# Optimization experiments

Hardware: AMD Instinct MI355X
Metric: run time of the kernel (lower is better)

The kernel has to match this reference:

```python
import jax, jax.numpy as jnp
import numpy as np

B, S, D = 2, 2048, 2048
H, HD = 16, 128


def _rope_cos_sin(seq_len, head_dim, base=10000.0):
    inv_freq = 1.0 / (base ** (np.arange(0, head_dim, 2, dtype=np.float32) / head_dim))
    t = np.arange(seq_len, dtype=np.float32)
    freqs = np.outer(t, inv_freq)                      # [S, HD/2]
    emb = np.concatenate([freqs, freqs], axis=-1)      # [S, HD]
    return jnp.asarray(np.cos(emb)), jnp.asarray(np.sin(emb))


def setup_inputs() -> dict:
    key = jax.random.key(0)
    k1, k2, k3 = jax.random.split(key, 3)
    hidden_states = jax.random.normal(k1, (B, S, D), dtype=jnp.float32)
    cos, sin = _rope_cos_sin(S, HD)
    # qkv weight: [3, H*HD, D] as in CastedLinear(batch_output_dims=(3,))
    w_qkv = jax.random.normal(k2, (3, H * HD, D), dtype=jnp.float32) * (1.0 / D ** 0.5)
    w_o = jax.random.normal(k3, (D, H * HD), dtype=jnp.float32) * (1.0 / (H * HD) ** 0.5)
    return {"hidden_states": hidden_states, "cos": cos, "sin": sin, "w_qkv": w_qkv, "w_o": w_o}


def _rotate_half(x):
    x1, x2 = jnp.split(x, 2, axis=-1)
    return jnp.concatenate([-x2, x1], axis=-1)


def _apply_rope(x, cos, sin):
    # x: [B, S, H, HD]; cos/sin: [S, HD] -> broadcast over heads via [:, None, :]
    return x * cos[:, None, :] + _rotate_half(x) * sin[:, None, :]


def reference(hidden_states, cos, sin, w_qkv, w_o):
    # fused QKV projection: weight flattened to [3*H*HD, D]
    qkv = jnp.einsum('bsd,fd->bsf', hidden_states, w_qkv.reshape(-1, D))  # [B,S,3*H*HD]
    # rearrange '... (h hd) -> ... h hd' with h=H  ->  [B,S,H,3*HD], then chunk
    qkv = qkv.reshape(B, S, H, 3 * HD)
    q, k, v = jnp.split(qkv, 3, axis=-1)          # each [B,S,H,HD]
    q = _apply_rope(q, cos, sin)
    k = _apply_rope(k, cos, sin)
    # SDPA, causal
    scale = 1.0 / jnp.sqrt(jnp.asarray(HD, dtype=q.dtype))
    scores = jnp.einsum('bshd,bthd->bhst', q, k) * scale      # [B,H,S,S]
    causal = jnp.tril(jnp.ones((S, S), dtype=bool))
    scores = jnp.where(causal, scores, jnp.asarray(-jnp.inf, dtype=scores.dtype))
    probs = jax.nn.softmax(scores, axis=-1)
    attn = jnp.einsum('bhst,bthd->bshd', probs, v)            # [B,S,H,HD]
    attn = attn.reshape(B, S, H * HD)
    return jnp.einsum('bsf,df->bsd', attn, w_o)               # [B,S,D]
```

## Files before the change

### kernel.cpp

```cpp
#include <hip/hip_runtime.h>

typedef unsigned short u16;
typedef __bf16 bf16x8 __attribute__((ext_vector_type(8)));
typedef float f32x4 __attribute__((ext_vector_type(4)));


__device__ __forceinline__ u16 f2bf(float x) {
  __bf16 h = (__bf16)x;
  return __builtin_bit_cast(u16, h);
}

__device__ __forceinline__ void async_copy16(void* lds, const void* g) {
  __builtin_amdgcn_global_load_lds((const __attribute__((address_space(1))) void*)g,
                                   (__attribute__((address_space(3))) void*)lds, 16, 0, 0);
}

__global__ __launch_bounds__(256) void cast_all(const float* __restrict__ hidden,
                                                const float* __restrict__ wqkv,
                                                const float* __restrict__ wo,
                                                u16* __restrict__ xb,
                                                u16* __restrict__ wqb,
                                                u16* __restrict__ wob) {
  int i = blockIdx.x * 256 + threadIdx.x;
  const float* s;
  u16* d;
  int off;
  if (i < 2097152) { s = hidden; d = xb; off = i; }
  else if (i < 2097152 + 3145728) { s = wqkv; d = wqb; off = i - 2097152; }
  else { s = wo; d = wob; off = i - (2097152 + 3145728); }
  float4 v = ((const float4*)s)[off];
  ushort4 o;
  o.x = f2bf(v.x); o.y = f2bf(v.y); o.z = f2bf(v.z); o.w = f2bf(v.w);
  ((ushort4*)d)[off] = o;
}

__global__ __launch_bounds__(256) void gemm_qkv(const u16* __restrict__ A,
                                                const u16* __restrict__ W,
                                                const float* __restrict__ cosb,
                                                const float* __restrict__ sinb,
                                                u16* __restrict__ Qb,
                                                u16* __restrict__ Kb,
                                                u16* __restrict__ Vt) {
  __shared__ __align__(16) u16 As[128 * 64];
  __shared__ __align__(16) u16 Bs[128 * 64];
  const int tid = threadIdx.x;
  const int lane = tid & 63;
  const int wave = tid >> 6;
  const int wm = (wave >> 1) * 64;
  const int r16 = lane & 15;
  const int g4 = lane >> 4;
  const int rsw = r16 & 7;
  const int bm = blockIdx.x * 128;
  const int bn = blockIdx.y * 128;

  size_t aoff[4], boff[4];
  u16* ldsA[4];
  u16* ldsB[4];
#pragma unroll
  for (int i = 0; i < 4; i++) {
    int row = wave * 32 + i * 8 + (lane >> 3);
    int c = (lane & 7) ^ (row & 7);
    aoff[i] = (size_t)(bm + row) * 2048 + c * 8;
    boff[i] = (size_t)(bn + row) * 2048 + c * 8;
    ldsA[i] = &As[(wave * 4 + i) * 512];
    ldsB[i] = &Bs[(wave * 4 + i) * 512];
  }

  int bcol[4];
#pragma unroll
  for (int n = 0; n < 4; n++) bcol[n] = (wave & 1) * 32 + (n & 1) * 16 + (n >> 1) * 64;

  f32x4 acc[4][4];
  f32x4 zero = {0.0f, 0.0f, 0.0f, 0.0f};
#pragma unroll
  for (int m = 0; m < 4; m++)
#pragma unroll
    for (int n = 0; n < 4; n++) acc[m][n] = zero;

  for (int kt = 0; kt < 2048; kt += 64) {
    __syncthreads();
#pragma unroll
    for (int i = 0; i < 4; i++) {
      async_copy16(ldsA[i], A + aoff[i] + kt);
      async_copy16(ldsB[i], W + boff[i] + kt);
    }
    __syncthreads();
#pragma unroll
    for (int ks = 0; ks < 2; ks++) {
      bf16x8 af[4], bfr[4];
#pragma unroll
      for (int m = 0; m < 4; m++)
        af[m] = *(const bf16x8*)(&As[(wm + m * 16 + r16) * 64 + ((ks * 4 + g4) ^ rsw) * 8]);
#pragma unroll
      for (int n = 0; n < 4; n++)
        bfr[n] = *(const bf16x8*)(&Bs[(bcol[n] + r16) * 64 + ((ks * 4 + g4) ^ rsw) * 8]);
#pragma unroll
      for (int m = 0; m < 4; m++)
#pragma unroll
        for (int n = 0; n < 4; n++)
          acc[m][n] = __builtin_amdgcn_mfma_f32_16x16x32_bf16(af[m], bfr[n], acc[m][n], 0, 0, 0);
    }
  }

  const int which = blockIdx.y % 3;
  const int hh = blockIdx.y / 3;
  const float qs = (which == 0) ? 0.08838834764831845f * 1.4426950408889634f : 1.0f;
#pragma unroll
  for (int m = 0; m < 4; m++) {
#pragma unroll
    for (int r = 0; r < 4; r++) {
      int row = bm + wm + m * 16 + g4 * 4 + r;
      int bb = row >> 11;
      int s = row & 2047;
      size_t bhIdx = (size_t)(bb * 16 + hh);
      if (which == 2) {
#pragma unroll
        for (int n = 0; n < 4; n++) {
          int hd = bcol[n] + r16;
          Vt[(bhIdx * 128 + hd) * 2048 + s] = f2bf(acc[m][n][r]);
        }
      } else {
        u16* dst = (which ? Kb : Qb) + (bhIdx * 2048 + s) * 128;
#pragma unroll
        for (int n = 0; n < 2; n++) {
          int hd = bcol[n] + r16;
          float c = cosb[s * 128 + hd] * qs;
          float sn = sinb[s * 128 + hd] * qs;
          float x1 = acc[m][n][r], x2 = acc[m][n + 2][r];
          dst[hd] = f2bf(x1 * c - x2 * sn);
          dst[hd + 64] = f2bf(x2 * c + x1 * sn);
        }
      }
    }
  }
}

__global__ __launch_bounds__(256) void flash_attn(const u16* __restrict__ Q,
                                                  const u16* __restrict__ K,
                                                  const u16* __restrict__ Vt,
                                                  u16* __restrict__ O) {
  __shared__ __align__(16) u16 Ks[128 * 128];
  __shared__ __align__(16) u16 Vs[128 * 128];
  __shared__ __align__(16) u16 Ps[4 * 16 * 72];
  const int tid = threadIdx.x;
  const int lane = tid & 63;
  const int wave = tid >> 6;
  const int bh = blockIdx.y;
  const int r16 = lane & 15;
  const int g4 = lane >> 4;
  const int rsw = r16 & 7;
  const u16* Qh = Q + (size_t)bh * 2048 * 128;
  const u16* Kh = K + (size_t)bh * 2048 * 128;
  const u16* Vh = Vt + (size_t)bh * 128 * 2048;
  const int b = bh >> 4;
  const int h = bh & 15;

  int koff[8], voff[8], ldsOff[8];
#pragma unroll
  for (int i = 0; i < 8; i++) {
    int r = (wave * 8 + i) * 4 + (lane >> 4);
    int c = (lane & 15) ^ (r & 7);
    koff[i] = r * 128 + c * 8;
    voff[i] = r * 2048 + c * 8;
    ldsOff[i] = (wave * 8 + i) * 512;
  }

#pragma unroll 1
  for (int pass = 0; pass < 2; pass++) {
    const int t = pass == 0 ? (int)blockIdx.x : 31 - (int)blockIdx.x;
    const int qg = t * 64 + wave * 16 + r16;
    const int nk = t / 2 + 1;

    bf16x8 qf[4];
#pragma unroll
    for (int ks = 0; ks < 4; ks++)
      qf[ks] = *(const bf16x8*)(Qh + (size_t)qg * 128 + ks * 32 + g4 * 8);

    f32x4 o[8];
    f32x4 zero = {0.0f, 0.0f, 0.0f, 0.0f};
#pragma unroll
    for (int c = 0; c < 8; c++) o[c] = zero;
    float m_i = -__builtin_inff();
    float l_i = 0.0f;

    for (int u = 0; u < nk; u++) {
      __syncthreads();
#pragma unroll
      for (int i = 0; i < 8; i++) {
        async_copy16(&Ks[ldsOff[i]], Kh + (size_t)u * 16384 + koff[i]);
        async_copy16(&Vs[ldsOff[i]], Vh + (size_t)u * 128 + voff[i]);
      }
      __syncthreads();

      f32x4 sacc[8];
#pragma unroll
      for (int n = 0; n < 8; n++) sacc[n] = zero;
#pragma unroll
      for (int n = 0; n < 8; n++) {
#pragma unroll
        for (int ks = 0; ks < 4; ks++) {
          bf16x8 kf = *(const bf16x8*)(&Ks[(n * 16 + r16) * 128 + ((ks * 4 + g4) ^ rsw) * 8]);
          sacc[n] = __builtin_amdgcn_mfma_f32_16x16x32_bf16(kf, qf[ks], sacc[n], 0, 0, 0);
        }
      }

      if (u == nk - 1) {
#pragma unroll
        for (int n = 0; n < 8; n++)
#pragma unroll
          for (int r = 0; r < 4; r++) {
            int key = u * 128 + 16 * n + g4 * 4 + r;
            if (key > qg) sacc[n][r] = -__builtin_inff();
          }
      }
      float vmax = -__builtin_inff();
#pragma unroll
      for (int n = 0; n < 8; n++)
#pragma unroll
        for (int r = 0; r < 4; r++) vmax = fmaxf(vmax, sacc[n][r]);
      vmax = fmaxf(vmax, __shfl_xor(vmax, 16));
      vmax = fmaxf(vmax, __shfl_xor(vmax, 32));
      float mn = fmaxf(m_i, vmax);
      float alpha = exp2f(m_i - mn);
      m_i = mn;

#pragma unroll
      for (int c = 0; c < 8; c++)
#pragma unroll
        for (int r = 0; r < 4; r++) o[c][r] *= alpha;

      float ssum = 0.0f;
      u16* Pw = &Ps[wave * 16 * 72];
#pragma unroll
      for (int half = 0; half < 2; half++) {
#pragma unroll
        for (int nl = 0; nl < 4; nl++) {
          int n = half * 4 + nl;
          float p0 = exp2f(sacc[n][0] - mn);
          float p1 = exp2f(sacc[n][1] - mn);
          float p2 = exp2f(sacc[n][2] - mn);
          float p3 = exp2f(sacc[n][3] - mn);
          ssum += (p0 + p1) + (p2 + p3);
          ushort4 pk;
          pk.x = f2bf(p0); pk.y = f2bf(p1); pk.z = f2bf(p2); pk.w = f2bf(p3);
          *(ushort4*)(&Pw[r16 * 72 + 16 * nl + g4 * 4]) = pk;
        }
#pragma unroll
        for (int ks2 = 0; ks2 < 2; ks2++) {
          bf16x8 pf = *(const bf16x8*)(&Pw[r16 * 72 + ks2 * 32 + g4 * 8]);
          int kv = half * 2 + ks2;
#pragma unroll
          for (int c = 0; c < 8; c++) {
            bf16x8 vf = *(const bf16x8*)(&Vs[(c * 16 + r16) * 128 + ((kv * 4 + g4) ^ rsw) * 8]);
            o[c] = __builtin_amdgcn_mfma_f32_16x16x32_bf16(vf, pf, o[c], 0, 0, 0);
          }
        }
      }
      ssum += __shfl_xor(ssum, 16);
      ssum += __shfl_xor(ssum, 32);
      l_i = l_i * alpha + ssum;
    }

    float rl = 1.0f / l_i;
    u16* dst = O + ((size_t)(b * 2048 + qg)) * 2048 + h * 128;
#pragma unroll
    for (int c = 0; c < 8; c++) {
      ushort4 pk;
      pk.x = f2bf(o[c][0] * rl);
      pk.y = f2bf(o[c][1] * rl);
      pk.z = f2bf(o[c][2] * rl);
      pk.w = f2bf(o[c][3] * rl);
      *(ushort4*)(dst + c * 16 + g4 * 4) = pk;
    }
  }
}

__global__ __launch_bounds__(256) void gemm_out(const u16* __restrict__ A,
                                                const u16* __restrict__ W,
                                                float* __restrict__ out) {
  __shared__ __align__(16) u16 As[128 * 64];
  __shared__ __align__(16) u16 Bs[128 * 64];
  const int tid = threadIdx.x;
  const int lane = tid & 63;
  const int wave = tid >> 6;
  const int wm = (wave >> 1) * 64;
  const int wn = (wave & 1) * 64;
  const int r16 = lane & 15;
  const int g4 = lane >> 4;
  const int rsw = r16 & 7;
  const int bm = blockIdx.x * 128;
  const int bn = blockIdx.y * 128;

  size_t aoff[4], boff[4];
  u16* ldsA[4];
  u16* ldsB[4];
#pragma unroll
  for (int i = 0; i < 4; i++) {
    int row = wave * 32 + i * 8 + (lane >> 3);
    int c = (lane & 7) ^ (row & 7);
    aoff[i] = (size_t)(bm + row) * 2048 + c * 8;
    boff[i] = (size_t)(bn + row) * 2048 + c * 8;
    ldsA[i] = &As[(wave * 4 + i) * 512];
    ldsB[i] = &Bs[(wave * 4 + i) * 512];
  }

  f32x4 acc[4][4];
  f32x4 zero = {0.0f, 0.0f, 0.0f, 0.0f};
#pragma unroll
  for (int m = 0; m < 4; m++)
#pragma unroll
    for (int n = 0; n < 4; n++) acc[m][n] = zero;

  for (int kt = 0; kt < 2048; kt += 64) {
    __syncthreads();
#pragma unroll
    for (int i = 0; i < 4; i++) {
      async_copy16(ldsA[i], A + aoff[i] + kt);
      async_copy16(ldsB[i], W + boff[i] + kt);
    }
    __syncthreads();
#pragma unroll
    for (int ks = 0; ks < 2; ks++) {
      bf16x8 af[4], bfr[4];
#pragma unroll
      for (int m = 0; m < 4; m++)
        af[m] = *(const bf16x8*)(&As[(wm + m * 16 + r16) * 64 + ((ks * 4 + g4) ^ rsw) * 8]);
#pragma unroll
      for (int n = 0; n < 4; n++)
        bfr[n] = *(const bf16x8*)(&Bs[(wn + n * 16 + r16) * 64 + ((ks * 4 + g4) ^ rsw) * 8]);
#pragma unroll
      for (int m = 0; m < 4; m++)
#pragma unroll
        for (int n = 0; n < 4; n++)
          acc[m][n] = __builtin_amdgcn_mfma_f32_16x16x32_bf16(af[m], bfr[n], acc[m][n], 0, 0, 0);
    }
  }

#pragma unroll
  for (int m = 0; m < 4; m++) {
#pragma unroll
    for (int n = 0; n < 4; n++) {
#pragma unroll
      for (int r = 0; r < 4; r++) {
        int row = bm + wm + m * 16 + g4 * 4 + r;
        int col = bn + wn + n * 16 + r16;
        out[(size_t)row * 2048 + col] = acc[m][n][r];
      }
    }
  }
}

extern "C" void kernel_launch(void* const* d_in, const int* in_sizes, int n_in,
                              void* d_out, int out_size, void* d_ws, size_t ws_size,
                              hipStream_t stream) {
  const float* hidden = (const float*)d_in[0];
  const float* cosb   = (const float*)d_in[1];
  const float* sinb   = (const float*)d_in[2];
  const float* w_qkv  = (const float*)d_in[3];
  const float* w_o    = (const float*)d_in[4];
  float* out = (float*)d_out;

  char* ws = (char*)d_ws;
  u16* Xbf    = (u16*)(ws);
  u16* Wqkvbf = (u16*)(ws + 16777216);
  u16* Wobf   = (u16*)(ws + 41943040);
  u16* Qb     = (u16*)(ws + 50331648);
  u16* Kb     = (u16*)(ws + 67108864);
  u16* Vt     = (u16*)(ws + 83886080);
  u16* Ob     = (u16*)(ws + 100663296);

  cast_all<<<24576, 256, 0, stream>>>(hidden, w_qkv, w_o, Xbf, Wqkvbf, Wobf);
  gemm_qkv<<<dim3(32, 48), 256, 0, stream>>>(Xbf, Wqkvbf, cosb, sinb, Qb, Kb, Vt);
  flash_attn<<<dim3(16, 32), 256, 0, stream>>>(Qb, Kb, Vt, Ob);
  gemm_out<<<dim3(32, 16), 256, 0, stream>>>(Ob, Wobf, out);
}
```

Before: 409.7 us.

## Double-buffer K/V tiles in flash attention with 8-wave 128-row query blocks

Restructures the flash attention kernel to 512 threads, each block covering 128 query rows, with two LDS buffers each for K and V. The next K/V tile is prefetched asynchronously while the current one is consumed, which removes the second barrier and should hide global-load latency behind the MFMA work. The P scratch buffer moves from padded rows to an XOR-swizzled layout to avoid LDS bank conflicts. The cost is roughly 144KB of LDS per block, so only one block fits per CU, and the grid halves to 256 blocks.

```diff
diff --git a/kernel.cpp b/kernel.cpp
--- a/kernel.cpp
+++ b/kernel.cpp
@@ -135,13 +135,13 @@
   }
 }
 
-__global__ __launch_bounds__(256) void flash_attn(const u16* __restrict__ Q,
+__global__ __launch_bounds__(512) void flash_attn(const u16* __restrict__ Q,
                                                   const u16* __restrict__ K,
                                                   const u16* __restrict__ Vt,
                                                   u16* __restrict__ O) {
-  __shared__ __align__(16) u16 Ks[128 * 128];
-  __shared__ __align__(16) u16 Vs[128 * 128];
-  __shared__ __align__(16) u16 Ps[4 * 16 * 72];
+  __shared__ __align__(16) u16 Ks[2][128 * 128];
+  __shared__ __align__(16) u16 Vs[2][128 * 128];
+  __shared__ __align__(16) u16 Ps[8 * 16 * 64];
   const int tid = threadIdx.x;
   const int lane = tid & 63;
   const int wave = tid >> 6;
@@ -155,21 +155,21 @@
   const int b = bh >> 4;
   const int h = bh & 15;
 
-  int koff[8], voff[8], ldsOff[8];
-#pragma unroll
-  for (int i = 0; i < 8; i++) {
-    int r = (wave * 8 + i) * 4 + (lane >> 4);
+  int koff[4], voff[4], ldsOff[4];
+#pragma unroll
+  for (int i = 0; i < 4; i++) {
+    int r = (wave * 4 + i) * 4 + (lane >> 4);
     int c = (lane & 15) ^ (r & 7);
     koff[i] = r * 128 + c * 8;
     voff[i] = r * 2048 + c * 8;
-    ldsOff[i] = (wave * 8 + i) * 512;
+    ldsOff[i] = (wave * 4 + i) * 512;
   }
 
 #pragma unroll 1
   for (int pass = 0; pass < 2; pass++) {
-    const int t = pass == 0 ? (int)blockIdx.x : 31 - (int)blockIdx.x;
-    const int qg = t * 64 + wave * 16 + r16;
-    const int nk = t / 2 + 1;
+    const int T = pass == 0 ? (int)blockIdx.x : 15 - (int)blockIdx.x;
+    const int qg = T * 128 + wave * 16 + r16;
+    const int nk = T + 1;
 
     bf16x8 qf[4];
 #pragma unroll
@@ -183,14 +183,23 @@
     float m_i = -__builtin_inff();
     float l_i = 0.0f;
 
+    __syncthreads();
+#pragma unroll
+    for (int i = 0; i < 4; i++) {
+      async_copy16(&Ks[0][ldsOff[i]], Kh + koff[i]);
+      async_copy16(&Vs[0][ldsOff[i]], Vh + voff[i]);
+    }
+
+    int cur = 0;
     for (int u = 0; u < nk; u++) {
       __syncthreads();
-#pragma unroll
-      for (int i = 0; i < 8; i++) {
-        async_copy16(&Ks[ldsOff[i]], Kh + (size_t)u * 16384 + koff[i]);
-        async_copy16(&Vs[ldsOff[i]], Vh + (size_t)u * 128 + voff[i]);
-      }
-      __syncthreads();
+      if (u + 1 < nk) {
+#pragma unroll
+        for (int i = 0; i < 4; i++) {
+          async_copy16(&Ks[cur ^ 1][ldsOff[i]], Kh + (size_t)(u + 1) * 16384 + koff[i]);
+          async_copy16(&Vs[cur ^ 1][ldsOff[i]], Vh + (size_t)(u + 1) * 128 + voff[i]);
+        }
+      }
 
       f32x4 sacc[8];
 #pragma unroll
@@ -199,7 +208,7 @@
       for (int n = 0; n < 8; n++) {
 #pragma unroll
         for (int ks = 0; ks < 4; ks++) {
-          bf16x8 kf = *(const bf16x8*)(&Ks[(n * 16 + r16) * 128 + ((ks * 4 + g4) ^ rsw) * 8]);
+          bf16x8 kf = *(const bf16x8*)(&Ks[cur][(n * 16 + r16) * 128 + ((ks * 4 + g4) ^ rsw) * 8]);
           sacc[n] = __builtin_amdgcn_mfma_f32_16x16x32_bf16(kf, qf[ks], sacc[n], 0, 0, 0);
         }
       }
@@ -230,7 +239,7 @@
         for (int r = 0; r < 4; r++) o[c][r] *= alpha;
 
       float ssum = 0.0f;
-      u16* Pw = &Ps[wave * 16 * 72];
+      u16* Pw = &Ps[wave * 1024];
 #pragma unroll
       for (int half = 0; half < 2; half++) {
 #pragma unroll
@@ -243,15 +252,15 @@
           ssum += (p0 + p1) + (p2 + p3);
           ushort4 pk;
           pk.x = f2bf(p0); pk.y = f2bf(p1); pk.z = f2bf(p2); pk.w = f2bf(p3);
-          *(ushort4*)(&Pw[r16 * 72 + 16 * nl + g4 * 4]) = pk;
+          *(ushort4*)(&Pw[r16 * 64 + ((2 * nl + (g4 >> 1)) ^ rsw) * 8 + (g4 & 1) * 4]) = pk;
         }
 #pragma unroll
         for (int ks2 = 0; ks2 < 2; ks2++) {
-          bf16x8 pf = *(const bf16x8*)(&Pw[r16 * 72 + ks2 * 32 + g4 * 8]);
+          bf16x8 pf = *(const bf16x8*)(&Pw[r16 * 64 + ((ks2 * 4 + g4) ^ rsw) * 8]);
           int kv = half * 2 + ks2;
 #pragma unroll
           for (int c = 0; c < 8; c++) {
-            bf16x8 vf = *(const bf16x8*)(&Vs[(c * 16 + r16) * 128 + ((kv * 4 + g4) ^ rsw) * 8]);
+            bf16x8 vf = *(const bf16x8*)(&Vs[cur][(c * 16 + r16) * 128 + ((kv * 4 + g4) ^ rsw) * 8]);
             o[c] = __builtin_amdgcn_mfma_f32_16x16x32_bf16(vf, pf, o[c], 0, 0, 0);
           }
         }
@@ -259,6 +268,7 @@
       ssum += __shfl_xor(ssum, 16);
       ssum += __shfl_xor(ssum, 32);
       l_i = l_i * alpha + ssum;
+      cur ^= 1;
     }
 
     float rl = 1.0f / l_i;
@@ -371,6 +381,6 @@
 
   cast_all<<<24576, 256, 0, stream>>>(hidden, w_qkv, w_o, Xbf, Wqkvbf, Wobf);
   gemm_qkv<<<dim3(32, 48), 256, 0, stream>>>(Xbf, Wqkvbf, cosb, sinb, Qb, Kb, Vt);
-  flash_attn<<<dim3(16, 32), 256, 0, stream>>>(Qb, Kb, Vt, Ob);
+  flash_attn<<<dim3(8, 32), 512, 0, stream>>>(Qb, Kb, Vt, Ob);
   gemm_out<<<dim3(32, 16), 256, 0, stream>>>(Ob, Wobf, out);
 }
```

Measured after the change: 396.4 us. -3.2%, faster.
